# Kernel optimization log

Hardware: AMD Instinct MI355X
Metric: run time of the kernel (lower is better)

The kernel has to match this reference:

```python
import jax, jax.numpy as jnp
import numpy as np

SIGMA_DATA = 16.0
ALPHA_BOND = 1.0


def safe_norm(x, axis=-1):
    # L2 norm with zero (sub)gradient at 0, matching torch.norm's behavior
    sq = jnp.sum(x * x, axis=axis)
    n = jnp.sqrt(jnp.where(sq > 0, sq, 1.0))
    return jnp.where(sq > 0, n, 0.0)


def weighted_rigid_align(x_l, xGT_l, w_l):
    # Aligns x_l onto xGT_l's frame (Kabsch with weights); output is detached.
    wm = w_l[..., None]                                   # [B,N,1]
    denom = jnp.sum(wm, axis=1, keepdims=True)
    mu = jnp.sum(wm * x_l, axis=1, keepdims=True) / denom
    muGT = jnp.sum(wm * xGT_l, axis=1, keepdims=True) / denom
    xc = x_l - mu
    xGTc = xGT_l - muGT
    # M = (w * xGT_c)^T @ x_c  -> [B,3,3]
    M = jnp.einsum('bni,bnj->bij', wm * xGTc, xc)
    U, S, Vh = jnp.linalg.svd(M)
    R = U @ Vh
    det = jnp.linalg.det(R)
    Fm = jnp.array([[1.0, 0.0, 0.0], [0.0, 1.0, 0.0], [0.0, 0.0, -1.0]], dtype=R.dtype)
    Rfix = jnp.einsum('bij,jk,bkl->bil', U, Fm, Vh)
    R = jnp.where(det[:, None, None] < 0, Rfix, R)
    xalign = xc @ jnp.swapaxes(R, -1, -2) + muGT
    return jax.lax.stop_gradient(xalign)


def diffusion_loss(xpred_l, xGT_l, ht, w_l):
    # Align ground truth onto prediction (note arg order in original forward)
    xGT_aligned = weighted_rigid_align(xGT_l, xpred_l, w_l)
    loss = jnp.sum(safe_norm(xpred_l - xGT_aligned) * w_l) / jnp.sum(w_l)
    if ALPHA_BOND > 0:
        w_pair = w_l[:, :, None] * w_l[:, None, :]                 # [B,N,N]
        d_pred = safe_norm(xpred_l[:, :, None] - xpred_l[:, None]) # [B,N,N]
        d_gt = safe_norm(xGT_l[:, :, None] - xGT_l[:, None])       # [B,N,N]
        L_bond = w_pair * (d_pred - d_gt) ** 2
        loss = loss + ALPHA_BOND * jnp.sum(L_bond) / jnp.sum(w_pair)
    return (ht ** 2 + SIGMA_DATA ** 2) / (ht + SIGMA_DATA) ** 2 * loss


def setup_inputs() -> dict:
    key = jax.random.key(0)
    k1, k2, k3, k4 = jax.random.split(key, 4)
    B, N = 4, 2048
    xpred_l = jax.random.normal(k1, (B, N, 3), dtype=jnp.float32) * 10.0
    xGT_l = jax.random.normal(k2, (B, N, 3), dtype=jnp.float32) * 10.0
    ht = jax.random.uniform(k3, (B,), dtype=jnp.float32, minval=0.1, maxval=4.0)
    w_l = jax.random.uniform(k4, (B, N), dtype=jnp.float32, minval=0.1, maxval=1.0)
    return {"xpred_l": xpred_l, "xGT_l": xGT_l, "ht": ht, "w_l": w_l}


def reference(xpred_l, xGT_l, ht, w_l):
    return diffusion_loss(xpred_l, xGT_l, ht, w_l)
```

## Files before the change

### kernel.cpp

```cpp
#include <hip/hip_runtime.h>
#include <math.h>


#define RT 256
#define CT 64

__global__ void k_stats(const float* __restrict__ pred, const float* __restrict__ gt,
                        const float* __restrict__ w, double* __restrict__ ws, int N) {
    int b = blockIdx.x;
    const float* p  = pred + (size_t)b * N * 3;
    const float* g  = gt   + (size_t)b * N * 3;
    const float* wb = w    + (size_t)b * N;

    double acc[16];
    #pragma unroll
    for (int i = 0; i < 16; i++) acc[i] = 0.0;

    for (int n = threadIdx.x; n < N; n += blockDim.x) {
        double wn = wb[n];
        double px = p[3*n], py = p[3*n+1], pz = p[3*n+2];
        double gx = g[3*n], gy = g[3*n+1], gz = g[3*n+2];
        acc[0] += wn;
        acc[1] += wn*px; acc[2] += wn*py; acc[3] += wn*pz;
        acc[4] += wn*gx; acc[5] += wn*gy; acc[6] += wn*gz;
        acc[7]  += wn*px*gx; acc[8]  += wn*px*gy; acc[9]  += wn*px*gz;
        acc[10] += wn*py*gx; acc[11] += wn*py*gy; acc[12] += wn*py*gz;
        acc[13] += wn*pz*gx; acc[14] += wn*pz*gy; acc[15] += wn*pz*gz;
    }

    #pragma unroll
    for (int off = 32; off > 0; off >>= 1) {
        #pragma unroll
        for (int i = 0; i < 16; i++) acc[i] += __shfl_down(acc[i], off, 64);
    }

    __shared__ double sh[4][16];
    int wave = threadIdx.x >> 6, lane = threadIdx.x & 63;
    if (lane == 0) {
        #pragma unroll
        for (int i = 0; i < 16; i++) sh[wave][i] = acc[i];
    }
    __syncthreads();
    if (threadIdx.x == 0) {
        int nw = blockDim.x >> 6;
        for (int i = 0; i < 16; i++) {
            double s = 0.0;
            for (int wv = 0; wv < nw; wv++) s += sh[wv][i];
            ws[b * 16 + i] = s;
        }
    }
}

__global__ void k_svd(double* __restrict__ ws, int B) {
    int b = threadIdx.x;
    if (b == 0) { ws[32*B] = 0.0; ws[32*B + 1] = 0.0; }
    if (b >= B) return;

    const double* s = ws + b * 16;
    double W = s[0];
    double mup[3] = { s[1]/W, s[2]/W, s[3]/W };
    double mug[3] = { s[4]/W, s[5]/W, s[6]/W };
    double M[3][3];
    for (int i = 0; i < 3; i++)
        for (int j = 0; j < 3; j++)
            M[i][j] = s[7 + i*3 + j] - W * mup[i] * mug[j];

    double A[3][3];
    for (int i = 0; i < 3; i++)
        for (int j = 0; j < 3; j++) {
            double t = 0.0;
            for (int k = 0; k < 3; k++) t += M[k][i] * M[k][j];
            A[i][j] = t;
        }

    double V[3][3] = {{1,0,0},{0,1,0},{0,0,1}};
    for (int sweep = 0; sweep < 12; sweep++) {
        for (int pq = 0; pq < 3; pq++) {
            int p = (pq == 2) ? 1 : 0;
            int q = (pq == 0) ? 1 : 2;
            double apq = A[p][q];
            if (fabs(apq) < 1e-300) continue;
            double app = A[p][p], aqq = A[q][q];
            double theta = (aqq - app) / (2.0 * apq);
            double t = copysign(1.0, theta) / (fabs(theta) + sqrt(theta*theta + 1.0));
            double c = 1.0 / sqrt(t*t + 1.0), sn = t * c;
            A[p][p] = app - t * apq;
            A[q][q] = aqq + t * apq;
            A[p][q] = A[q][p] = 0.0;
            int r = 3 - p - q;
            double arp = A[r][p], arq = A[r][q];
            A[r][p] = A[p][r] = c*arp - sn*arq;
            A[r][q] = A[q][r] = sn*arp + c*arq;
            for (int rr = 0; rr < 3; rr++) {
                double vp = V[rr][p], vq = V[rr][q];
                V[rr][p] = c*vp - sn*vq;
                V[rr][q] = sn*vp + c*vq;
            }
        }
    }
    double d[3] = { A[0][0], A[1][1], A[2][2] };

    int idx[3] = {0, 1, 2};
    for (int i = 0; i < 2; i++)
        for (int j = i + 1; j < 3; j++)
            if (d[idx[j]] > d[idx[i]]) { int tt = idx[i]; idx[i] = idx[j]; idx[j] = tt; }

    double u[3][3], v[3][3];
    for (int i = 0; i < 3; i++) {
        int c_ = idx[i];
        double sv = sqrt(fmax(d[c_], 0.0));
        double inv = (sv > 1e-12) ? 1.0 / sv : 0.0;
        for (int r = 0; r < 3; r++) v[i][r] = V[r][c_];
        for (int r = 0; r < 3; r++) {
            double t = 0.0;
            for (int k = 0; k < 3; k++) t += M[r][k] * v[i][k];
            u[i][r] = t * inv;
        }
    }

    double detM = M[0][0]*(M[1][1]*M[2][2] - M[1][2]*M[2][1])
                - M[0][1]*(M[1][0]*M[2][2] - M[1][2]*M[2][0])
                + M[0][2]*(M[1][0]*M[2][1] - M[1][1]*M[2][0]);
    double sg2 = (detM < 0.0) ? -1.0 : 1.0;

    double* o = ws + 16*B + b*16;
    for (int r = 0; r < 3; r++)
        for (int cc = 0; cc < 3; cc++)
            o[r*3 + cc] = u[0][r]*v[0][cc] + u[1][r]*v[1][cc] + sg2 * u[2][r]*v[2][cc];
    for (int i = 0; i < 3; i++) o[9 + i]  = mup[i];
    for (int i = 0; i < 3; i++) o[12 + i] = mug[i];
    o[15] = W;
}

__global__ void k_pair(const float* __restrict__ pred, const float* __restrict__ gt,
                       const float* __restrict__ w, double* __restrict__ ws,
                       int N, int B) {
    int b  = blockIdx.z;
    int n  = blockIdx.x * RT + threadIdx.x;
    int c0 = blockIdx.y * CT;
    const float* p  = pred + (size_t)b * N * 3;
    const float* g  = gt   + (size_t)b * N * 3;
    const float* wb = w    + (size_t)b * N;

    __shared__ float sp[CT][3], sg[CT][3], sw[CT];
    for (int i = threadIdx.x; i < CT; i += blockDim.x) {
        int m = c0 + i;
        if (m < N) {
            sp[i][0] = p[3*m]; sp[i][1] = p[3*m+1]; sp[i][2] = p[3*m+2];
            sg[i][0] = g[3*m]; sg[i][1] = g[3*m+1]; sg[i][2] = g[3*m+2];
            sw[i] = wb[m];
        } else {
            sp[i][0] = sp[i][1] = sp[i][2] = 0.0f;
            sg[i][0] = sg[i][1] = sg[i][2] = 0.0f;
            sw[i] = 0.0f;
        }
    }
    __syncthreads();

    float  bond_f  = 0.0f;
    double align_d = 0.0;
    if (n < N) {
        float px = p[3*n], py = p[3*n+1], pz = p[3*n+2];
        float gx = g[3*n], gy = g[3*n+1], gz = g[3*n+2];
        float wn = wb[n];
        int cc = min(CT, N - c0);
        for (int i = 0; i < cc; i++) {
            float dxp = px - sp[i][0], dyp = py - sp[i][1], dzp = pz - sp[i][2];
            float dp  = sqrtf(dxp*dxp + dyp*dyp + dzp*dzp);
            float dxg = gx - sg[i][0], dyg = gy - sg[i][1], dzg = gz - sg[i][2];
            float dg  = sqrtf(dxg*dxg + dyg*dyg + dzg*dzg);
            float dd  = dp - dg;
            bond_f += wn * sw[i] * dd * dd;
        }
        if (blockIdx.y == 0) {
            const double* o = ws + 16*B + b*16;
            double xc0 = (double)gx - o[12], xc1 = (double)gy - o[13], xc2 = (double)gz - o[14];
            double ax = o[0]*xc0 + o[1]*xc1 + o[2]*xc2 + o[9];
            double ay = o[3]*xc0 + o[4]*xc1 + o[5]*xc2 + o[10];
            double az = o[6]*xc0 + o[7]*xc1 + o[8]*xc2 + o[11];
            double ex = (double)px - ax, ey = (double)py - ay, ez = (double)pz - az;
            double sq = ex*ex + ey*ey + ez*ez;
            align_d = (sq > 0.0) ? (double)wn * sqrt(sq) : 0.0;
        }
    }

    double bd = (double)bond_f;
    #pragma unroll
    for (int off = 32; off > 0; off >>= 1) {
        bd      += __shfl_down(bd, off, 64);
        align_d += __shfl_down(align_d, off, 64);
    }
    __shared__ double shb[4], sha[4];
    int wave = threadIdx.x >> 6, lane = threadIdx.x & 63;
    if (lane == 0) { shb[wave] = bd; sha[wave] = align_d; }
    __syncthreads();
    if (threadIdx.x == 0) {
        int nw = blockDim.x >> 6;
        double bt = 0.0, at = 0.0;
        for (int wv = 0; wv < nw; wv++) { bt += shb[wv]; at += sha[wv]; }
        if (at != 0.0) atomicAdd(&ws[32*B], at);
        atomicAdd(&ws[32*B + 1], bt);
    }
}

__global__ void k_final(const float* __restrict__ ht, const double* __restrict__ ws,
                        float* __restrict__ out, int B) {
    int b = threadIdx.x;
    if (b >= B) return;
    double tw = 0.0, twp = 0.0;
    for (int i = 0; i < B; i++) {
        double W = ws[16*B + i*16 + 15];
        tw  += W;
        twp += W * W;
    }
    double loss = ws[32*B] / tw + ws[32*B + 1] / twp;
    double h = ht[b];
    double scale = (h*h + 256.0) / ((h + 16.0) * (h + 16.0));
    out[b] = (float)(scale * loss);
}

extern "C" void kernel_launch(void* const* d_in, const int* in_sizes, int n_in,
                              void* d_out, int out_size, void* d_ws, size_t ws_size,
                              hipStream_t stream) {
    const float* pred = (const float*)d_in[0];
    const float* gt   = (const float*)d_in[1];
    const float* ht   = (const float*)d_in[2];
    const float* w    = (const float*)d_in[3];
    int B = in_sizes[2];
    int N = in_sizes[3] / B;
    double* ws = (double*)d_ws;
    float* out = (float*)d_out;

    k_stats<<<dim3(B), dim3(256), 0, stream>>>(pred, gt, w, ws, N);
    k_svd<<<dim3(1), dim3(64), 0, stream>>>(ws, B);
    dim3 g3((N + RT - 1) / RT, (N + CT - 1) / CT, B);
    k_pair<<<g3, dim3(RT), 0, stream>>>(pred, gt, w, ws, N, B);
    k_final<<<dim3(1), dim3(64), 0, stream>>>(ht, ws, out, B);
}
```

Measured before the change: 103.4 us.

## Fuse stats, SVD, pair and final kernels into one last-block-done kernel

Merges the four launches into a single kernel. Weighted statistics are accumulated with atomics from the first column-tile blocks, and the bond sum uses pair symmetry so only the upper triangle is computed and doubled. The last block to finish, detected by an atomic counter, runs the 3x3 SVD, the alignment residual over all points and the final scaling. This removes launch gaps and about half of the pairwise work, at the cost of a memset, atomic contention and a serial alignment pass over B*N points in one block.

```diff
diff --git a/kernel.cpp b/kernel.cpp
--- a/kernel.cpp
+++ b/kernel.cpp
@@ -4,219 +4,226 @@
 
 #define RT 256
 #define CT 64
-
-__global__ void k_stats(const float* __restrict__ pred, const float* __restrict__ gt,
-                        const float* __restrict__ w, double* __restrict__ ws, int N) {
-    int b = blockIdx.x;
+#define MAXB 8
+
+__global__ __launch_bounds__(RT, 4)
+void k_main(const float* __restrict__ pred, const float* __restrict__ gt,
+            const float* __restrict__ ht, const float* __restrict__ w,
+            float* __restrict__ out, double* __restrict__ ws,
+            int N, int B, unsigned total) {
+    const int b   = blockIdx.z;
+    const int r0  = blockIdx.x * RT;
+    const int c0  = blockIdx.y * CT;
+    const int tid = threadIdx.x;
+    const int lane = tid & 63, wave = tid >> 6;
     const float* p  = pred + (size_t)b * N * 3;
     const float* g  = gt   + (size_t)b * N * 3;
     const float* wb = w    + (size_t)b * N;
-
-    double acc[16];
-    #pragma unroll
-    for (int i = 0; i < 16; i++) acc[i] = 0.0;
-
-    for (int n = threadIdx.x; n < N; n += blockDim.x) {
-        double wn = wb[n];
-        double px = p[3*n], py = p[3*n+1], pz = p[3*n+2];
-        double gx = g[3*n], gy = g[3*n+1], gz = g[3*n+2];
-        acc[0] += wn;
-        acc[1] += wn*px; acc[2] += wn*py; acc[3] += wn*pz;
-        acc[4] += wn*gx; acc[5] += wn*gy; acc[6] += wn*gz;
-        acc[7]  += wn*px*gx; acc[8]  += wn*px*gy; acc[9]  += wn*px*gz;
-        acc[10] += wn*py*gx; acc[11] += wn*py*gy; acc[12] += wn*py*gz;
-        acc[13] += wn*pz*gx; acc[14] += wn*pz*gy; acc[15] += wn*pz*gz;
-    }
-
-    #pragma unroll
-    for (int off = 32; off > 0; off >>= 1) {
-        #pragma unroll
-        for (int i = 0; i < 16; i++) acc[i] += __shfl_down(acc[i], off, 64);
-    }
-
-    __shared__ double sh[4][16];
-    int wave = threadIdx.x >> 6, lane = threadIdx.x & 63;
-    if (lane == 0) {
-        #pragma unroll
-        for (int i = 0; i < 16; i++) sh[wave][i] = acc[i];
-    }
-    __syncthreads();
-    if (threadIdx.x == 0) {
-        int nw = blockDim.x >> 6;
-        for (int i = 0; i < 16; i++) {
-            double s = 0.0;
-            for (int wv = 0; wv < nw; wv++) s += sh[wv][i];
-            ws[b * 16 + i] = s;
-        }
-    }
-}
-
-__global__ void k_svd(double* __restrict__ ws, int B) {
-    int b = threadIdx.x;
-    if (b == 0) { ws[32*B] = 0.0; ws[32*B + 1] = 0.0; }
-    if (b >= B) return;
-
-    const double* s = ws + b * 16;
-    double W = s[0];
-    double mup[3] = { s[1]/W, s[2]/W, s[3]/W };
-    double mug[3] = { s[4]/W, s[5]/W, s[6]/W };
-    double M[3][3];
-    for (int i = 0; i < 3; i++)
-        for (int j = 0; j < 3; j++)
-            M[i][j] = s[7 + i*3 + j] - W * mup[i] * mug[j];
-
-    double A[3][3];
-    for (int i = 0; i < 3; i++)
-        for (int j = 0; j < 3; j++) {
-            double t = 0.0;
-            for (int k = 0; k < 3; k++) t += M[k][i] * M[k][j];
-            A[i][j] = t;
-        }
-
-    double V[3][3] = {{1,0,0},{0,1,0},{0,0,1}};
-    for (int sweep = 0; sweep < 12; sweep++) {
-        for (int pq = 0; pq < 3; pq++) {
-            int p = (pq == 2) ? 1 : 0;
-            int q = (pq == 0) ? 1 : 2;
-            double apq = A[p][q];
-            if (fabs(apq) < 1e-300) continue;
-            double app = A[p][p], aqq = A[q][q];
-            double theta = (aqq - app) / (2.0 * apq);
-            double t = copysign(1.0, theta) / (fabs(theta) + sqrt(theta*theta + 1.0));
-            double c = 1.0 / sqrt(t*t + 1.0), sn = t * c;
-            A[p][p] = app - t * apq;
-            A[q][q] = aqq + t * apq;
-            A[p][q] = A[q][p] = 0.0;
-            int r = 3 - p - q;
-            double arp = A[r][p], arq = A[r][q];
-            A[r][p] = A[p][r] = c*arp - sn*arq;
-            A[r][q] = A[q][r] = sn*arp + c*arq;
-            for (int rr = 0; rr < 3; rr++) {
-                double vp = V[rr][p], vq = V[rr][q];
-                V[rr][p] = c*vp - sn*vq;
-                V[rr][q] = sn*vp + c*vq;
-            }
-        }
-    }
-    double d[3] = { A[0][0], A[1][1], A[2][2] };
-
-    int idx[3] = {0, 1, 2};
-    for (int i = 0; i < 2; i++)
-        for (int j = i + 1; j < 3; j++)
-            if (d[idx[j]] > d[idx[i]]) { int tt = idx[i]; idx[i] = idx[j]; idx[j] = tt; }
-
-    double u[3][3], v[3][3];
-    for (int i = 0; i < 3; i++) {
-        int c_ = idx[i];
-        double sv = sqrt(fmax(d[c_], 0.0));
-        double inv = (sv > 1e-12) ? 1.0 / sv : 0.0;
-        for (int r = 0; r < 3; r++) v[i][r] = V[r][c_];
-        for (int r = 0; r < 3; r++) {
-            double t = 0.0;
-            for (int k = 0; k < 3; k++) t += M[r][k] * v[i][k];
-            u[i][r] = t * inv;
-        }
-    }
-
-    double detM = M[0][0]*(M[1][1]*M[2][2] - M[1][2]*M[2][1])
-                - M[0][1]*(M[1][0]*M[2][2] - M[1][2]*M[2][0])
-                + M[0][2]*(M[1][0]*M[2][1] - M[1][1]*M[2][0]);
-    double sg2 = (detM < 0.0) ? -1.0 : 1.0;
-
-    double* o = ws + 16*B + b*16;
-    for (int r = 0; r < 3; r++)
-        for (int cc = 0; cc < 3; cc++)
-            o[r*3 + cc] = u[0][r]*v[0][cc] + u[1][r]*v[1][cc] + sg2 * u[2][r]*v[2][cc];
-    for (int i = 0; i < 3; i++) o[9 + i]  = mup[i];
-    for (int i = 0; i < 3; i++) o[12 + i] = mug[i];
-    o[15] = W;
-}
-
-__global__ void k_pair(const float* __restrict__ pred, const float* __restrict__ gt,
-                       const float* __restrict__ w, double* __restrict__ ws,
-                       int N, int B) {
-    int b  = blockIdx.z;
-    int n  = blockIdx.x * RT + threadIdx.x;
-    int c0 = blockIdx.y * CT;
-    const float* p  = pred + (size_t)b * N * 3;
-    const float* g  = gt   + (size_t)b * N * 3;
-    const float* wb = w    + (size_t)b * N;
-
-    __shared__ float sp[CT][3], sg[CT][3], sw[CT];
-    for (int i = threadIdx.x; i < CT; i += blockDim.x) {
-        int m = c0 + i;
-        if (m < N) {
-            sp[i][0] = p[3*m]; sp[i][1] = p[3*m+1]; sp[i][2] = p[3*m+2];
-            sg[i][0] = g[3*m]; sg[i][1] = g[3*m+1]; sg[i][2] = g[3*m+2];
-            sw[i] = wb[m];
-        } else {
-            sp[i][0] = sp[i][1] = sp[i][2] = 0.0f;
-            sg[i][0] = sg[i][1] = sg[i][2] = 0.0f;
-            sw[i] = 0.0f;
-        }
-    }
-    __syncthreads();
-
-    float  bond_f  = 0.0f;
-    double align_d = 0.0;
-    if (n < N) {
-        float px = p[3*n], py = p[3*n+1], pz = p[3*n+2];
-        float gx = g[3*n], gy = g[3*n+1], gz = g[3*n+2];
-        float wn = wb[n];
+    double* stats = ws + (size_t)b * 16;
+    double* bondp = ws + 16 * B;
+    unsigned* cnt = (unsigned*)(ws + 16 * B + 1);
+
+    __shared__ float4 sp4[CT], sg4[CT];
+    __shared__ double shred[4][16];
+
+    const bool bond_active = (c0 + CT > r0 + 1);
+
+    const int n = r0 + tid;
+    const bool row_ok = (n < N);
+    float px=0.f,py=0.f,pz=0.f,gx=0.f,gy=0.f,gz=0.f,wn=0.f;
+    if (row_ok) {
+        px = p[3*n]; py = p[3*n+1]; pz = p[3*n+2];
+        gx = g[3*n]; gy = g[3*n+1]; gz = g[3*n+2];
+        wn = wb[n];
+    }
+
+    if (bond_active) {
+        for (int i = tid; i < CT; i += RT) {
+            int m = c0 + i;
+            if (m < N) {
+                sp4[i] = make_float4(p[3*m], p[3*m+1], p[3*m+2], wb[m]);
+                sg4[i] = make_float4(g[3*m], g[3*m+1], g[3*m+2], 0.0f);
+            } else {
+                sp4[i] = make_float4(0.f,0.f,0.f,0.f);
+                sg4[i] = make_float4(0.f,0.f,0.f,0.f);
+            }
+        }
+        __syncthreads();
+    }
+
+    float bond_f = 0.0f;
+    if (bond_active && row_ok && (c0 + CT - 1 > n)) {
         int cc = min(CT, N - c0);
         for (int i = 0; i < cc; i++) {
-            float dxp = px - sp[i][0], dyp = py - sp[i][1], dzp = pz - sp[i][2];
+            float4 cp = sp4[i];
+            float4 cg = sg4[i];
+            float dxp = px-cp.x, dyp = py-cp.y, dzp = pz-cp.z;
             float dp  = sqrtf(dxp*dxp + dyp*dyp + dzp*dzp);
-            float dxg = gx - sg[i][0], dyg = gy - sg[i][1], dzg = gz - sg[i][2];
+            float dxg = gx-cg.x, dyg = gy-cg.y, dzg = gz-cg.z;
             float dg  = sqrtf(dxg*dxg + dyg*dyg + dzg*dzg);
             float dd  = dp - dg;
-            bond_f += wn * sw[i] * dd * dd;
-        }
-        if (blockIdx.y == 0) {
-            const double* o = ws + 16*B + b*16;
-            double xc0 = (double)gx - o[12], xc1 = (double)gy - o[13], xc2 = (double)gz - o[14];
-            double ax = o[0]*xc0 + o[1]*xc1 + o[2]*xc2 + o[9];
-            double ay = o[3]*xc0 + o[4]*xc1 + o[5]*xc2 + o[10];
-            double az = o[6]*xc0 + o[7]*xc1 + o[8]*xc2 + o[11];
-            double ex = (double)px - ax, ey = (double)py - ay, ez = (double)pz - az;
-            double sq = ex*ex + ey*ey + ez*ez;
-            align_d = (sq > 0.0) ? (double)wn * sqrt(sq) : 0.0;
+            float t   = wn * cp.w * dd * dd;
+            bond_f += (c0 + i > n) ? t : 0.0f;
+        }
+    }
+    bond_f *= 2.0f;
+
+    if (blockIdx.y == 0) {
+        double wd = (double)wn;
+        double pxd=px, pyd=py, pzd=pz, gxd=gx, gyd=gy, gzd=gz;
+        double st[16];
+        st[0]=wd;
+        st[1]=wd*pxd;  st[2]=wd*pyd;  st[3]=wd*pzd;
+        st[4]=wd*gxd;  st[5]=wd*gyd;  st[6]=wd*gzd;
+        st[7]=wd*pxd*gxd;  st[8]=wd*pxd*gyd;  st[9]=wd*pxd*gzd;
+        st[10]=wd*pyd*gxd; st[11]=wd*pyd*gyd; st[12]=wd*pyd*gzd;
+        st[13]=wd*pzd*gxd; st[14]=wd*pzd*gyd; st[15]=wd*pzd*gzd;
+        #pragma unroll
+        for (int off = 32; off > 0; off >>= 1) {
+            #pragma unroll
+            for (int k = 0; k < 16; k++) st[k] += __shfl_down(st[k], off, 64);
+        }
+        if (lane == 0) {
+            #pragma unroll
+            for (int k = 0; k < 16; k++) shred[wave][k] = st[k];
+        }
+        __syncthreads();
+        if (tid < 16) {
+            double s = shred[0][tid]+shred[1][tid]+shred[2][tid]+shred[3][tid];
+            unsafeAtomicAdd(&stats[tid], s);
         }
     }
 
     double bd = (double)bond_f;
     #pragma unroll
-    for (int off = 32; off > 0; off >>= 1) {
-        bd      += __shfl_down(bd, off, 64);
-        align_d += __shfl_down(align_d, off, 64);
-    }
-    __shared__ double shb[4], sha[4];
-    int wave = threadIdx.x >> 6, lane = threadIdx.x & 63;
-    if (lane == 0) { shb[wave] = bd; sha[wave] = align_d; }
-    __syncthreads();
-    if (threadIdx.x == 0) {
-        int nw = blockDim.x >> 6;
-        double bt = 0.0, at = 0.0;
-        for (int wv = 0; wv < nw; wv++) { bt += shb[wv]; at += sha[wv]; }
-        if (at != 0.0) atomicAdd(&ws[32*B], at);
-        atomicAdd(&ws[32*B + 1], bt);
-    }
-}
-
-__global__ void k_final(const float* __restrict__ ht, const double* __restrict__ ws,
-                        float* __restrict__ out, int B) {
-    int b = threadIdx.x;
-    if (b >= B) return;
-    double tw = 0.0, twp = 0.0;
-    for (int i = 0; i < B; i++) {
-        double W = ws[16*B + i*16 + 15];
-        tw  += W;
-        twp += W * W;
-    }
-    double loss = ws[32*B] / tw + ws[32*B + 1] / twp;
-    double h = ht[b];
-    double scale = (h*h + 256.0) / ((h + 16.0) * (h + 16.0));
-    out[b] = (float)(scale * loss);
+    for (int off = 32; off > 0; off >>= 1) bd += __shfl_down(bd, off, 64);
+    __syncthreads();
+    if (lane == 0) shred[wave][0] = bd;
+    __syncthreads();
+    if (tid == 0) {
+        double bt = shred[0][0]+shred[1][0]+shred[2][0]+shred[3][0];
+        unsafeAtomicAdd(bondp, bt);
+    }
+
+    __shared__ int s_last;
+    __syncthreads();
+    if (tid == 0) {
+        __threadfence();
+        unsigned old = atomicAdd(cnt, 1u);
+        s_last = (old == total - 1u) ? 1 : 0;
+    }
+    __syncthreads();
+    if (!s_last) return;
+
+    __shared__ double Rm[MAXB][16];
+    if (tid < B) {
+        double s[16];
+        double* sb = ws + (size_t)tid * 16;
+        for (int k = 0; k < 16; k++) s[k] = unsafeAtomicAdd(&sb[k], 0.0);
+        double W = s[0];
+        double mup[3] = { s[1]/W, s[2]/W, s[3]/W };
+        double mug[3] = { s[4]/W, s[5]/W, s[6]/W };
+        double M[3][3];
+        for (int i = 0; i < 3; i++)
+            for (int j = 0; j < 3; j++)
+                M[i][j] = s[7 + i*3 + j] - W * mup[i] * mug[j];
+
+        double A[3][3];
+        for (int i = 0; i < 3; i++)
+            for (int j = 0; j < 3; j++) {
+                double t = 0.0;
+                for (int k = 0; k < 3; k++) t += M[k][i] * M[k][j];
+                A[i][j] = t;
+            }
+        double V[3][3] = {{1,0,0},{0,1,0},{0,0,1}};
+        for (int sweep = 0; sweep < 8; sweep++) {
+            for (int pq = 0; pq < 3; pq++) {
+                int pp_ = (pq == 2) ? 1 : 0;
+                int qq_ = (pq == 0) ? 1 : 2;
+                double apq = A[pp_][qq_];
+                if (fabs(apq) < 1e-300) continue;
+                double app = A[pp_][pp_], aqq = A[qq_][qq_];
+                double theta = (aqq - app) / (2.0 * apq);
+                double t = copysign(1.0, theta) / (fabs(theta) + sqrt(theta*theta + 1.0));
+                double c = 1.0 / sqrt(t*t + 1.0), sn = t * c;
+                A[pp_][pp_] = app - t * apq;
+                A[qq_][qq_] = aqq + t * apq;
+                A[pp_][qq_] = A[qq_][pp_] = 0.0;
+                int r = 3 - pp_ - qq_;
+                double arp = A[r][pp_], arq = A[r][qq_];
+                A[r][pp_] = A[pp_][r] = c*arp - sn*arq;
+                A[r][qq_] = A[qq_][r] = sn*arp + c*arq;
+                for (int rr = 0; rr < 3; rr++) {
+                    double vp = V[rr][pp_], vq = V[rr][qq_];
+                    V[rr][pp_] = c*vp - sn*vq;
+                    V[rr][qq_] = sn*vp + c*vq;
+                }
+            }
+        }
+        double d[3] = { A[0][0], A[1][1], A[2][2] };
+        int idx[3] = {0, 1, 2};
+        for (int i = 0; i < 2; i++)
+            for (int j = i + 1; j < 3; j++)
+                if (d[idx[j]] > d[idx[i]]) { int tt = idx[i]; idx[i] = idx[j]; idx[j] = tt; }
+        double u[3][3], v[3][3];
+        for (int i = 0; i < 3; i++) {
+            int c_ = idx[i];
+            double sv = sqrt(fmax(d[c_], 0.0));
+            double inv = (sv > 1e-12) ? 1.0 / sv : 0.0;
+            for (int r = 0; r < 3; r++) v[i][r] = V[r][c_];
+            for (int r = 0; r < 3; r++) {
+                double t = 0.0;
+                for (int k = 0; k < 3; k++) t += M[r][k] * v[i][k];
+                u[i][r] = t * inv;
+            }
+        }
+        double detM = M[0][0]*(M[1][1]*M[2][2] - M[1][2]*M[2][1])
+                    - M[0][1]*(M[1][0]*M[2][2] - M[1][2]*M[2][0])
+                    + M[0][2]*(M[1][0]*M[2][1] - M[1][1]*M[2][0]);
+        double sg2 = (detM < 0.0) ? -1.0 : 1.0;
+        double* o = Rm[tid];
+        for (int r = 0; r < 3; r++)
+            for (int cc2 = 0; cc2 < 3; cc2++)
+                o[r*3 + cc2] = u[0][r]*v[0][cc2] + u[1][r]*v[1][cc2] + sg2 * u[2][r]*v[2][cc2];
+        for (int i = 0; i < 3; i++) o[9 + i]  = mup[i];
+        for (int i = 0; i < 3; i++) o[12 + i] = mug[i];
+        o[15] = W;
+    }
+    __syncthreads();
+
+    double al = 0.0;
+    for (int idx2 = tid; idx2 < B * N; idx2 += RT) {
+        int bb = idx2 / N, nn = idx2 - bb * N;
+        const float* pp = pred + ((size_t)bb * N + nn) * 3;
+        const float* gg = gt   + ((size_t)bb * N + nn) * 3;
+        double wv = w[(size_t)bb * N + nn];
+        const double* o = Rm[bb];
+        double xc0 = (double)gg[0]-o[12], xc1 = (double)gg[1]-o[13], xc2 = (double)gg[2]-o[14];
+        double ax = o[0]*xc0 + o[1]*xc1 + o[2]*xc2 + o[9];
+        double ay = o[3]*xc0 + o[4]*xc1 + o[5]*xc2 + o[10];
+        double az = o[6]*xc0 + o[7]*xc1 + o[8]*xc2 + o[11];
+        double ex = (double)pp[0]-ax, ey = (double)pp[1]-ay, ez = (double)pp[2]-az;
+        double sq = ex*ex + ey*ey + ez*ez;
+        al += (sq > 0.0) ? wv * sqrt(sq) : 0.0;
+    }
+    #pragma unroll
+    for (int off = 32; off > 0; off >>= 1) al += __shfl_down(al, off, 64);
+    __syncthreads();
+    if (lane == 0) shred[wave][1] = al;
+    __syncthreads();
+    __shared__ double s_loss;
+    if (tid == 0) {
+        double at = shred[0][1]+shred[1][1]+shred[2][1]+shred[3][1];
+        double tw = 0.0, twp = 0.0;
+        for (int i = 0; i < B; i++) { double W = Rm[i][15]; tw += W; twp += W*W; }
+        double bond = unsafeAtomicAdd(bondp, 0.0);
+        s_loss = at / tw + bond / twp;
+    }
+    __syncthreads();
+    if (tid < B) {
+        double h = (double)ht[tid];
+        out[tid] = (float)(((h*h + 256.0) / ((h + 16.0)*(h + 16.0))) * s_loss);
+    }
 }
 
 extern "C" void kernel_launch(void* const* d_in, const int* in_sizes, int n_in,
@@ -231,9 +238,9 @@
     double* ws = (double*)d_ws;
     float* out = (float*)d_out;
 
-    k_stats<<<dim3(B), dim3(256), 0, stream>>>(pred, gt, w, ws, N);
-    k_svd<<<dim3(1), dim3(64), 0, stream>>>(ws, B);
-    dim3 g3((N + RT - 1) / RT, (N + CT - 1) / CT, B);
-    k_pair<<<g3, dim3(RT), 0, stream>>>(pred, gt, w, ws, N, B);
-    k_final<<<dim3(1), dim3(64), 0, stream>>>(ht, ws, out, B);
+    hipMemsetAsync(d_ws, 0, (size_t)(16 * B + 2) * sizeof(double), stream);
+
+    dim3 grid((N + RT - 1) / RT, (N + CT - 1) / CT, B);
+    unsigned total = grid.x * grid.y * grid.z;
+    k_main<<<grid, dim3(RT), 0, stream>>>(pred, gt, ht, w, out, ws, N, B, total);
 }
```

New measurement: 107.7 us. +4.1%, slower.
